# Performance work log

Hardware: AMD Instinct MI355X
Metric: run time of the kernel (lower is better)

The kernel has to match this reference:

```python
import jax, jax.numpy as jnp
import numpy as np

B, D, L = 4, 512, 4096
N1, N2 = 1167, 8921


def setup_inputs() -> dict:
    key = jax.random.key(0)
    k1, k2, k3, k4 = jax.random.split(key, 4)
    H = jax.random.normal(k1, (B, D, L), dtype=jnp.float32)
    Q1_w = jax.random.normal(k2, (N1, D), dtype=jnp.float32) * (1.0 / np.sqrt(D))
    Q2_w = jax.random.normal(k3, (N2, D), dtype=jnp.float32) * (1.0 / np.sqrt(D))
    Q12_w = jax.random.normal(k4, (N2, N1), dtype=jnp.float32) * (1.0 / np.sqrt(N1))
    return {"H": H, "Q1_w": Q1_w, "Q2_w": Q2_w, "Q12_w": Q12_w}


def reference(H, Q1_w, Q2_w, Q12_w):
    # H: [b, d, l]; Q1_w: [n1, d]; Q2_w: [n2, d]; Q12_w: [n2, n1]
    # Level-1 label attention
    E1 = jnp.einsum('nd,bdl->bnl', Q1_w, H)          # [b, n1, l]
    A1 = jax.nn.softmax(E1, axis=2)
    C1 = jnp.einsum('bnl,bdl->bnd', A1, H)           # [b, n1, d]
    # Project level-1 context to level-2 label space
    C1 = jnp.einsum('mn,bnd->bmd', Q12_w, C1)        # [b, n2, d]
    # Level-2 queries modulated by level-1 context (elementwise)
    Q2 = Q2_w[None, :, :] * C1                       # [b, n2, d]
    E2 = jnp.einsum('bmd,bdl->bml', Q2, H)           # [b, n2, l]
    A2 = jax.nn.softmax(E2, axis=2)
    C2 = jnp.einsum('bml,bdl->bmd', A2, H)           # [b, n2, d]
    return (C2, A2)
```

## Files before the change

kernel.cpp:

```cpp
#include <hip/hip_runtime.h>
#include <hip/hip_bf16.h>

typedef __bf16 bf16_t;
typedef __bf16 bf16x8 __attribute__((ext_vector_type(8)));
typedef __bf16 bf16x4 __attribute__((ext_vector_type(4)));
typedef float  f32x4  __attribute__((ext_vector_type(4)));

#define BM 128
#define BN 128
#define BK 64

#define SBAR() asm volatile("s_barrier" ::: "memory")

__global__ __launch_bounds__(256) void cast_transpose_H(
    const float* __restrict__ H, bf16_t* __restrict__ Hb,
    bf16_t* __restrict__ HTb, int D, int L) {
  __shared__ bf16_t tile[32][33];
  int b = blockIdx.z;
  int l0 = blockIdx.x * 32, d0 = blockIdx.y * 32;
  const float* Hp = H + (size_t)b * D * L;
  bf16_t* Hbp = Hb + (size_t)b * D * L;
  bf16_t* HTp = HTb + (size_t)b * L * D;
  int tx = threadIdx.x, ty = threadIdx.y;
#pragma unroll
  for (int r = 0; r < 4; r++) {
    int d = d0 + ty + r * 8;
    float v = Hp[(size_t)d * L + l0 + tx];
    bf16_t bv = (bf16_t)v;
    tile[ty + r * 8][tx] = bv;
    Hbp[(size_t)d * L + l0 + tx] = bv;
  }
  __syncthreads();
#pragma unroll
  for (int r = 0; r < 4; r++) {
    int l = l0 + ty + r * 8;
    HTp[(size_t)l * D + d0 + tx] = tile[tx][ty + r * 8];
  }
}

__global__ void cast_w(const float* __restrict__ in, bf16_t* __restrict__ out, int n) {
  int i = blockIdx.x * 256 + threadIdx.x;
  if (i < n) out[i] = (bf16_t)in[i];
}

__global__ void cast_w_pad(const float* __restrict__ in, bf16_t* __restrict__ out,
                           int cols, int ldo) {
  int c = blockIdx.x * 256 + threadIdx.x;
  int r = blockIdx.y;
  if (c < ldo) {
    float v = (c < cols) ? in[(size_t)r * cols + c] : 0.0f;
    out[(size_t)r * ldo + c] = (bf16_t)v;
  }
}

__global__ void zero_rows(bf16_t* __restrict__ p, int r0, int nr, long sb, int L) {
  long i = (long)blockIdx.x * 256 + threadIdx.x;
  int b = blockIdx.y;
  long tot = (long)nr * L / 8;
  if (i < tot) {
    bf16x8 z = {};
    *(bf16x8*)(p + ((long)b * sb + r0) * L + i * 8) = z;
  }
}

__device__ inline bf16x8 cvt8(float4 a, float4 b) {
  bf16x8 o;
  o[0] = (bf16_t)a.x; o[1] = (bf16_t)a.y; o[2] = (bf16_t)a.z; o[3] = (bf16_t)a.w;
  o[4] = (bf16_t)b.x; o[5] = (bf16_t)b.y; o[6] = (bf16_t)b.z; o[7] = (bf16_t)b.w;
  return o;
}

__device__ inline void gload_lds16(const bf16_t* g, bf16_t* l) {
  __builtin_amdgcn_global_load_lds(
      (const __attribute__((address_space(1))) void*)g,
      (__attribute__((address_space(3))) void*)l, 16, 0, 0);
}

__device__ inline void stage_half(const bf16_t* __restrict__ src, int ld,
                                  bf16_t* lds_half, int t, int wid) {
  int r = t >> 3;
  int gsl = (t & 7) ^ (r & 7);
  const bf16_t* g = src + (size_t)r * ld + gsl * 8;
  gload_lds16(g, lds_half + wid * 512);
  gload_lds16(g + (size_t)64 * ld, lds_half + 4096 + wid * 512);
}

template <int EPI>
__global__ __launch_bounds__(512) void gemm256_bt(
    const bf16_t* __restrict__ A, long sAb, const bf16_t* __restrict__ BT, long sBb,
    void* __restrict__ Cv, long sCb, const float* __restrict__ W,
    int M, int N, int K, int lda, int ldb, int ldc) {
  __shared__ __align__(16) bf16_t As[2][256][64];
  __shared__ __align__(16) bf16_t Bs[2][256][64];
  int b = blockIdx.z;
  A += (size_t)b * sAb;
  BT += (size_t)b * sBb;

  int nx = gridDim.x, ny = gridDim.y;
  int nwg = nx * ny;
  int bid = blockIdx.x + nx * blockIdx.y;
  int qq = nwg >> 3, rr = nwg & 7;
  int xcd = bid & 7, lin = bid >> 3;
  int swz = (xcd < rr ? xcd * (qq + 1) : rr * (qq + 1) + (xcd - rr) * qq) + lin;
  int m0 = (swz / ny) * 256;
  int n0 = (swz % ny) * 256;

  int t = threadIdx.x;
  int lane = t & 63, wid = t >> 6;
  int l15 = lane & 15, q = lane >> 4;
  int wm = (wid >> 2) * 128;
  int wn = (wid & 3) * 64;
  int NT = K >> 6;

  f32x4 acc[8][4];
#pragma unroll
  for (int i = 0; i < 8; i++)
#pragma unroll
    for (int j = 0; j < 4; j++)
#pragma unroll
      for (int e = 0; e < 4; e++) acc[i][j][e] = 0.0f;

  stage_half(BT + (size_t)(n0 + 0) * ldb, ldb, &Bs[0][0][0], t, wid);
  stage_half(BT + (size_t)(n0 + 128) * ldb, ldb, &Bs[0][128][0], t, wid);
  stage_half(A + (size_t)(m0 + 0) * lda, lda, &As[0][0][0], t, wid);
  stage_half(A + (size_t)(m0 + 128) * lda, lda, &As[0][128][0], t, wid);
  stage_half(BT + (size_t)(n0 + 0) * ldb + 64, ldb, &Bs[1][0][0], t, wid);
  stage_half(BT + (size_t)(n0 + 128) * ldb + 64, ldb, &Bs[1][128][0], t, wid);
  asm volatile("s_waitcnt vmcnt(4)" ::: "memory");
  SBAR();

  bf16x8 af[4][2];
  bf16x8 bF[2][2][2];

  for (int kt = 0; kt < NT; ++kt) {
    int buf = kt & 1;
    const bf16_t* An = A + (size_t)m0 * lda + (size_t)(kt + 1) * 64;
    const bf16_t* Bn2 = BT + (size_t)n0 * ldb + (size_t)(kt + 2) * 64;

    auto readA = [&](int mh) {
#pragma unroll
      for (int i = 0; i < 4; i++) {
        const char* rowp = (const char*)&As[buf][wm + mh * 64 + i * 16 + l15][0];
#pragma unroll
        for (int ks = 0; ks < 2; ks++)
          af[i][ks] = *(const bf16x8*)(rowp + ((((ks * 4 + q) ^ (l15 & 7))) << 4));
      }
    };
    auto readB = [&](int ch) {
#pragma unroll
      for (int j = 0; j < 2; j++) {
        const char* rowp = (const char*)&Bs[buf][wn + ch * 32 + j * 16 + l15][0];
#pragma unroll
        for (int ks = 0; ks < 2; ks++)
          bF[ch][j][ks] = *(const bf16x8*)(rowp + ((((ks * 4 + q) ^ (l15 & 7))) << 4));
      }
    };
    auto mmaq = [&](int mh, int ch) {
      __builtin_amdgcn_s_setprio(1);
#pragma unroll
      for (int i = 0; i < 4; i++)
#pragma unroll
        for (int j = 0; j < 2; j++)
#pragma unroll
          for (int ks = 0; ks < 2; ks++)
            acc[mh * 4 + i][ch * 2 + j] = __builtin_amdgcn_mfma_f32_16x16x32_bf16(
                af[i][ks], bF[ch][j][ks], acc[mh * 4 + i][ch * 2 + j], 0, 0, 0);
      __builtin_amdgcn_s_setprio(0);
    };

    readA(0);
    readB(0);
    if (kt + 1 < NT) stage_half(An, lda, &As[buf ^ 1][0][0], t, wid);
    SBAR();
    mmaq(0, 0);
    SBAR();
    readB(1);
    if (kt + 1 < NT) stage_half(An + (size_t)128 * lda, lda, &As[buf ^ 1][128][0], t, wid);
    SBAR();
    mmaq(0, 1);
    SBAR();
    readA(1);
    if (kt + 2 < NT) stage_half(Bn2, ldb, &Bs[buf][0][0], t, wid);
    SBAR();
    mmaq(1, 0);
    SBAR();
    if (kt + 2 < NT) {
      stage_half(Bn2 + (size_t)128 * ldb, ldb, &Bs[buf][128][0], t, wid);
      asm volatile("s_waitcnt vmcnt(4)" ::: "memory");
    } else if (kt + 1 < NT) {
      asm volatile("s_waitcnt vmcnt(0)" ::: "memory");
    }
    SBAR();
    mmaq(1, 1);
    SBAR();
  }

#pragma unroll
  for (int ig = 0; ig < 8; ig++) {
    int rbase = m0 + wm + ig * 16 + q * 4;
#pragma unroll
    for (int jg = 0; jg < 4; jg++) {
      int c = n0 + wn + jg * 16 + l15;
#pragma unroll
      for (int r4 = 0; r4 < 4; r4++) {
        int r = rbase + r4;
        if (r < M) {
          float val = acc[ig][jg][r4];
          ((float*)Cv + (size_t)b * sCb)[(size_t)r * ldc + c] = val;
        }
      }
    }
  }
}

template <typename AT, int EPI>
__global__ __launch_bounds__(256) void gemm_bt(
    const AT* __restrict__ A, long sAb, const bf16_t* __restrict__ BT, long sBb,
    void* __restrict__ Cv, long sCb, const float* __restrict__ W,
    int M, int N, int K, int lda, int ldb, int ldc) {
  constexpr bool AF32 = (sizeof(AT) == 4);
  __shared__ __align__(16) bf16_t As[BM][BK];
  __shared__ __align__(16) bf16_t Bs[BN][BK];
  int b = blockIdx.z;
  A += (size_t)b * sAb;
  BT += (size_t)b * sBb;

  int nx = gridDim.x, ny = gridDim.y;
  int nwg = nx * ny;
  int bid = blockIdx.x + nx * blockIdx.y;
  int qq = nwg >> 3, rr = nwg & 7;
  int xcd = bid & 7, lin = bid >> 3;
  int swz = (xcd < rr ? xcd * (qq + 1) : rr * (qq + 1) + (xcd - rr) * qq) + lin;
  int m0 = (swz / ny) * BM;
  int n0 = (swz % ny) * BN;

  int t = threadIdx.x;
  int lane = t & 63, wid = t >> 6;
  int l15 = lane & 15, q = lane >> 4;
  int wm = (wid >> 1) * 64, wn = (wid & 1) * 64;

  int r0 = t >> 3;
  int sl = t & 7;
  int gsl = sl ^ (r0 & 7);
  bf16_t* lA = &As[0][0] + (size_t)wid * 512;
  bf16_t* lB = &Bs[0][0] + (size_t)wid * 512;

  f32x4 acc[4][4];
#pragma unroll
  for (int i = 0; i < 4; i++)
#pragma unroll
    for (int j = 0; j < 4; j++)
#pragma unroll
      for (int e = 0; e < 4; e++) acc[i][j][e] = 0.0f;

  for (int kb = 0; kb < K; kb += BK) {
    float4 va[4][2];
    if constexpr (AF32) {
#pragma unroll
      for (int i = 0; i < 4; i++) {
        int gm = m0 + i * 32 + r0;
        if (gm < M) {
          const float4* p = (const float4*)(A + (size_t)gm * lda + kb + gsl * 8);
          va[i][0] = p[0];
          va[i][1] = p[1];
        } else {
          va[i][0] = make_float4(0.f, 0.f, 0.f, 0.f);
          va[i][1] = make_float4(0.f, 0.f, 0.f, 0.f);
        }
      }
    }
    __syncthreads();
#pragma unroll
    for (int i = 0; i < 4; i++)
      gload_lds16(BT + (size_t)(n0 + i * 32 + r0) * ldb + kb + gsl * 8,
                  lB + i * 2048);
    if constexpr (AF32) {
#pragma unroll
      for (int i = 0; i < 4; i++)
        *(bf16x8*)(&As[0][0] + (size_t)(i * 256 + t) * 8) = cvt8(va[i][0], va[i][1]);
    } else {
#pragma unroll
      for (int i = 0; i < 4; i++)
        gload_lds16(A + (size_t)(m0 + i * 32 + r0) * lda + kb + gsl * 8,
                    lA + i * 2048);
    }
    __syncthreads();

#pragma unroll
    for (int ks = 0; ks < 2; ks++) {
      bf16x8 af[4], bfr[4];
#pragma unroll
      for (int i = 0; i < 4; i++) {
        int row = wm + i * 16 + l15;
        int off = (ks * 64 + q * 16) ^ ((l15 & 7) << 4);
        af[i] = *(const bf16x8*)((const char*)&As[row][0] + off);
      }
#pragma unroll
      for (int j = 0; j < 4; j++) {
        int row = wn + j * 16 + l15;
        int off = (ks * 64 + q * 16) ^ ((l15 & 7) << 4);
        bfr[j] = *(const bf16x8*)((const char*)&Bs[row][0] + off);
      }
#pragma unroll
      for (int i = 0; i < 4; i++)
#pragma unroll
        for (int j = 0; j < 4; j++)
          acc[i][j] = __builtin_amdgcn_mfma_f32_16x16x32_bf16(af[i], bfr[j],
                                                              acc[i][j], 0, 0, 0);
    }
  }

#pragma unroll
  for (int i = 0; i < 4; i++) {
    int rbase = m0 + wm + i * 16 + q * 4;
#pragma unroll
    for (int j = 0; j < 4; j++) {
      int c = n0 + wn + j * 16 + l15;
#pragma unroll
      for (int r4 = 0; r4 < 4; r4++) {
        int r = rbase + r4;
        if (r < M) {
          float val = acc[i][j][r4];
          if (EPI == 0) {
            float* Cp = (float*)Cv + (size_t)b * sCb;
            Cp[(size_t)r * ldc + c] = val;
          } else if (EPI == 2) {
            float w = W[(size_t)r * N + c];
            bf16_t* Cp = (bf16_t*)Cv + (size_t)b * sCb;
            Cp[(size_t)r * ldc + c] = (bf16_t)(val * w);
          } else {
            bf16_t* Cp = (bf16_t*)Cv + (size_t)b * sCb;
            Cp[(size_t)r * ldc + c] = (bf16_t)val;
          }
        }
      }
    }
  }
}

template <int MODE>
__global__ __launch_bounds__(256) void softmax_rows(
    const float* __restrict__ in, void* __restrict__ out,
    bf16_t* __restrict__ out2, int L, int ostr) {
  long row_in = (long)blockIdx.y * gridDim.x + blockIdx.x;
  long row_out = (long)blockIdx.y * ostr + blockIdx.x;
  const float* ip = in + row_in * L;
  int t = threadIdx.x;
  int lane = t & 63, wid = t >> 6;
  float4 v[4];
  float m = -3.4e38f;
#pragma unroll
  for (int c = 0; c < 4; c++) {
    v[c] = ((const float4*)ip)[c * 256 + t];
    m = fmaxf(m, fmaxf(fmaxf(v[c].x, v[c].y), fmaxf(v[c].z, v[c].w)));
  }
#pragma unroll
  for (int off = 1; off < 64; off <<= 1) m = fmaxf(m, __shfl_xor(m, off));
  __shared__ float redm[4];
  __shared__ float reds[4];
  if (lane == 0) redm[wid] = m;
  __syncthreads();
  m = fmaxf(fmaxf(redm[0], redm[1]), fmaxf(redm[2], redm[3]));
  float s = 0.0f;
#pragma unroll
  for (int c = 0; c < 4; c++) {
    v[c].x = __expf(v[c].x - m);
    v[c].y = __expf(v[c].y - m);
    v[c].z = __expf(v[c].z - m);
    v[c].w = __expf(v[c].w - m);
    s += (v[c].x + v[c].y) + (v[c].z + v[c].w);
  }
#pragma unroll
  for (int off = 1; off < 64; off <<= 1) s += __shfl_xor(s, off);
  if (lane == 0) reds[wid] = s;
  __syncthreads();
  s = (reds[0] + reds[1]) + (reds[2] + reds[3]);
  float inv = 1.0f / s;
  if (MODE == 1) {
    bf16_t* op = (bf16_t*)out + row_out * L;
#pragma unroll
    for (int c = 0; c < 4; c++) {
      bf16x4 o;
      o[0] = (bf16_t)(v[c].x * inv);
      o[1] = (bf16_t)(v[c].y * inv);
      o[2] = (bf16_t)(v[c].z * inv);
      o[3] = (bf16_t)(v[c].w * inv);
      *(bf16x4*)(op + ((size_t)c * 256 + t) * 4) = o;
    }
  } else {
    float* op = (float*)out + row_out * L;
#pragma unroll
    for (int c = 0; c < 4; c++) {
      float fx = v[c].x * inv, fy = v[c].y * inv, fz = v[c].z * inv, fw = v[c].w * inv;
      ((float4*)op)[c * 256 + t] = make_float4(fx, fy, fz, fw);
      if (MODE == 2) {
        bf16x4 o;
        o[0] = (bf16_t)fx; o[1] = (bf16_t)fy; o[2] = (bf16_t)fz; o[3] = (bf16_t)fw;
        *(bf16x4*)(out2 + row_out * L + ((size_t)c * 256 + t) * 4) = o;
      }
    }
  }
}

extern "C" void kernel_launch(void* const* d_in, const int* in_sizes, int n_in,
                              void* d_out, int out_size, void* d_ws, size_t ws_size,
                              hipStream_t stream) {
  const int B = 4, D = 512, L = 4096, N1 = 1167, N2 = 8921;
  const int N1P = 1280;
  const int M2P = 8960;
  const float* H = (const float*)d_in[0];
  const float* Q1w = (const float*)d_in[1];
  const float* Q2w = (const float*)d_in[2];
  const float* Q12w = (const float*)d_in[3];
  float* C2 = (float*)d_out;
  float* A2 = C2 + (size_t)B * N2 * D;

  char* ws = (char*)d_ws;
  size_t off = 0;
  auto alloc = [&](size_t bytes) -> void* {
    void* p = ws + off;
    off = (off + bytes + 255) & ~(size_t)255;
    return p;
  };
  bf16_t* Hb   = (bf16_t*)alloc((size_t)B * D * L * 2);
  bf16_t* HTb  = (bf16_t*)alloc((size_t)B * L * D * 2);
  bf16_t* Q1b  = (bf16_t*)alloc((size_t)N1P * D * 2);
  bf16_t* Q12b = (bf16_t*)alloc((size_t)M2P * N1P * 2);
  float*  E1   = (float*)alloc((size_t)B * N1 * L * 4);
  bf16_t* A1b  = (bf16_t*)alloc((size_t)B * N1P * L * 2);
  bf16_t* C1Tb = (bf16_t*)alloc((size_t)B * D * N1P * 2);
  bf16_t* Q2b  = (bf16_t*)alloc(((size_t)B * N2 + 64) * D * 2);
  size_t a2b_bytes = ((size_t)B * N2 + 128) * (size_t)L * 2;
  bool useA2b = (ws_size > 0) && (off + a2b_bytes <= ws_size);
  bf16_t* A2b = (bf16_t*)alloc(a2b_bytes);

  cast_transpose_H<<<dim3(L / 32, D / 32, B), dim3(32, 8), 0, stream>>>(H, Hb, HTb, D, L);
  cast_w_pad<<<dim3((D + 255) / 256, N1P), 256, 0, stream>>>(Q1w, Q1b, D, D);
  zero_rows<<<dim3(((N1P - N1) * D / 8 + 255) / 256, 1), 256, 0, stream>>>(
      Q1b, N1, N1P - N1, 0, D);
  cast_w_pad<<<dim3((N1P + 255) / 256, N2), 256, 0, stream>>>(Q12w, Q12b, N1, N1P);
  zero_rows<<<dim3(((N1P - N1) * L / 8 + 255) / 256, B), 256, 0, stream>>>(
      A1b, N1, N1P - N1, (long)N1P, L);
  gemm_bt<bf16_t, 0><<<dim3(N1P / BM, L / BN, B), 256, 0, stream>>>(
      Q1b, 0, HTb, (long)L * D, E1, (long)N1 * L, nullptr, N1, L, D, D, D, L);
  softmax_rows<1><<<dim3(N1, B), 256, 0, stream>>>(E1, A1b, nullptr, L, N1P);
  gemm_bt<bf16_t, 3><<<dim3(D / BM, N1P / BN, B), 256, 0, stream>>>(
      Hb, (long)D * L, A1b, (long)N1P * L, C1Tb, (long)D * N1P, nullptr,
      D, N1P, L, L, L, N1P);
  gemm_bt<bf16_t, 2><<<dim3(M2P / BM, D / BN, B), 256, 0, stream>>>(
      Q12b, 0, C1Tb, (long)D * N1P, Q2b, (long)N2 * D, Q2w, N2, D, N1P, N1P, N1P, D);
  gemm256_bt<0><<<dim3(M2P / 256, L / 256, B), 512, 0, stream>>>(
      Q2b, (long)N2 * D, HTb, (long)L * D, A2, (long)N2 * L, nullptr, N2, L, D, D, D, L);
  if (useA2b) {
    softmax_rows<2><<<dim3(B * N2, 1), 256, 0, stream>>>(A2, A2, A2b, L, 0);
    gemm_bt<bf16_t, 0><<<dim3(M2P / BM, D / BN, B), 256, 0, stream>>>(
        A2b, (long)N2 * L, Hb, (long)D * L, C2, (long)N2 * D, nullptr, N2, D, L, L, L, D);
  } else {
    softmax_rows<0><<<dim3(B * N2, 1), 256, 0, stream>>>(A2, A2, nullptr, L, 0);
    gemm_bt<float, 0><<<dim3(M2P / BM, D / BN, B), 256, 0, stream>>>(
        A2, (long)N2 * L, Hb, (long)D * L, C2, (long)N2 * D, nullptr, N2, D, L, L, L, D);
  }
}
```

Measured before the change: 1.649 ms.

## Use nontemporal stores/loads for A2 path and trim padded K in Q12 GEMM

Switches the large fp32 E2/A2 stores in the 256-tile GEMM and the MODE 2 softmax loads and stores to nontemporal variants, so streaming data does not pollute the cache. Reduces the K extent of the Q12 projection GEMM from the padded 1280 to 1216, skipping all-zero padding columns. Also casts only the real Q1 rows instead of the padded count and removes an unused kernel. Nontemporal hints can hurt if the A2 data would have been re-read from cache by the following softmax.

```diff
diff --git a/kernel.cpp b/kernel.cpp
--- a/kernel.cpp
+++ b/kernel.cpp
@@ -38,11 +38,6 @@
   }
 }
 
-__global__ void cast_w(const float* __restrict__ in, bf16_t* __restrict__ out, int n) {
-  int i = blockIdx.x * 256 + threadIdx.x;
-  if (i < n) out[i] = (bf16_t)in[i];
-}
-
 __global__ void cast_w_pad(const float* __restrict__ in, bf16_t* __restrict__ out,
                            int cols, int ldo) {
   int c = blockIdx.x * 256 + threadIdx.x;
@@ -206,7 +201,8 @@
         int r = rbase + r4;
         if (r < M) {
           float val = acc[ig][jg][r4];
-          ((float*)Cv + (size_t)b * sCb)[(size_t)r * ldc + c] = val;
+          float* Cp = (float*)Cv + (size_t)b * sCb;
+          __builtin_nontemporal_store(val, &Cp[(size_t)r * ldc + c]);
         }
       }
     }
@@ -347,12 +343,15 @@
   const float* ip = in + row_in * L;
   int t = threadIdx.x;
   int lane = t & 63, wid = t >> 6;
-  float4 v[4];
+  f32x4 v[4];
   float m = -3.4e38f;
 #pragma unroll
   for (int c = 0; c < 4; c++) {
-    v[c] = ((const float4*)ip)[c * 256 + t];
-    m = fmaxf(m, fmaxf(fmaxf(v[c].x, v[c].y), fmaxf(v[c].z, v[c].w)));
+    if (MODE == 2)
+      v[c] = __builtin_nontemporal_load((const f32x4*)ip + c * 256 + t);
+    else
+      v[c] = ((const f32x4*)ip)[c * 256 + t];
+    m = fmaxf(m, fmaxf(fmaxf(v[c][0], v[c][1]), fmaxf(v[c][2], v[c][3])));
   }
 #pragma unroll
   for (int off = 1; off < 64; off <<= 1) m = fmaxf(m, __shfl_xor(m, off));
@@ -364,11 +363,11 @@
   float s = 0.0f;
 #pragma unroll
   for (int c = 0; c < 4; c++) {
-    v[c].x = __expf(v[c].x - m);
-    v[c].y = __expf(v[c].y - m);
-    v[c].z = __expf(v[c].z - m);
-    v[c].w = __expf(v[c].w - m);
-    s += (v[c].x + v[c].y) + (v[c].z + v[c].w);
+    v[c][0] = __expf(v[c][0] - m);
+    v[c][1] = __expf(v[c][1] - m);
+    v[c][2] = __expf(v[c][2] - m);
+    v[c][3] = __expf(v[c][3] - m);
+    s += (v[c][0] + v[c][1]) + (v[c][2] + v[c][3]);
   }
 #pragma unroll
   for (int off = 1; off < 64; off <<= 1) s += __shfl_xor(s, off);
@@ -381,22 +380,25 @@
 #pragma unroll
     for (int c = 0; c < 4; c++) {
       bf16x4 o;
-      o[0] = (bf16_t)(v[c].x * inv);
-      o[1] = (bf16_t)(v[c].y * inv);
-      o[2] = (bf16_t)(v[c].z * inv);
-      o[3] = (bf16_t)(v[c].w * inv);
+      o[0] = (bf16_t)(v[c][0] * inv);
+      o[1] = (bf16_t)(v[c][1] * inv);
+      o[2] = (bf16_t)(v[c][2] * inv);
+      o[3] = (bf16_t)(v[c][3] * inv);
       *(bf16x4*)(op + ((size_t)c * 256 + t) * 4) = o;
     }
   } else {
     float* op = (float*)out + row_out * L;
 #pragma unroll
     for (int c = 0; c < 4; c++) {
-      float fx = v[c].x * inv, fy = v[c].y * inv, fz = v[c].z * inv, fw = v[c].w * inv;
-      ((float4*)op)[c * 256 + t] = make_float4(fx, fy, fz, fw);
+      f32x4 o = v[c] * inv;
       if (MODE == 2) {
-        bf16x4 o;
-        o[0] = (bf16_t)fx; o[1] = (bf16_t)fy; o[2] = (bf16_t)fz; o[3] = (bf16_t)fw;
-        *(bf16x4*)(out2 + row_out * L + ((size_t)c * 256 + t) * 4) = o;
+        __builtin_nontemporal_store(o, (f32x4*)op + c * 256 + t);
+        bf16x4 ob;
+        ob[0] = (bf16_t)o[0]; ob[1] = (bf16_t)o[1];
+        ob[2] = (bf16_t)o[2]; ob[3] = (bf16_t)o[3];
+        __builtin_nontemporal_store(ob, (bf16x4*)(out2 + row_out * L) + c * 256 + t);
+      } else {
+        ((f32x4*)op)[c * 256 + t] = o;
       }
     }
   }
@@ -407,6 +409,7 @@
                               hipStream_t stream) {
   const int B = 4, D = 512, L = 4096, N1 = 1167, N2 = 8921;
   const int N1P = 1280;
+  const int N1K = 1216;
   const int M2P = 8960;
   const float* H = (const float*)d_in[0];
   const float* Q1w = (const float*)d_in[1];
@@ -435,7 +438,7 @@
   bf16_t* A2b = (bf16_t*)alloc(a2b_bytes);
 
   cast_transpose_H<<<dim3(L / 32, D / 32, B), dim3(32, 8), 0, stream>>>(H, Hb, HTb, D, L);
-  cast_w_pad<<<dim3((D + 255) / 256, N1P), 256, 0, stream>>>(Q1w, Q1b, D, D);
+  cast_w_pad<<<dim3((D + 255) / 256, N1), 256, 0, stream>>>(Q1w, Q1b, D, D);
   zero_rows<<<dim3(((N1P - N1) * D / 8 + 255) / 256, 1), 256, 0, stream>>>(
       Q1b, N1, N1P - N1, 0, D);
   cast_w_pad<<<dim3((N1P + 255) / 256, N2), 256, 0, stream>>>(Q12w, Q12b, N1, N1P);
@@ -448,7 +451,7 @@
       Hb, (long)D * L, A1b, (long)N1P * L, C1Tb, (long)D * N1P, nullptr,
       D, N1P, L, L, L, N1P);
   gemm_bt<bf16_t, 2><<<dim3(M2P / BM, D / BN, B), 256, 0, stream>>>(
-      Q12b, 0, C1Tb, (long)D * N1P, Q2b, (long)N2 * D, Q2w, N2, D, N1P, N1P, N1P, D);
+      Q12b, 0, C1Tb, (long)D * N1P, Q2b, (long)N2 * D, Q2w, N2, D, N1K, N1P, N1P, D);
   gemm256_bt<0><<<dim3(M2P / 256, L / 256, B), 512, 0, stream>>>(
       Q2b, (long)N2 * D, HTb, (long)L * D, A2, (long)N2 * L, nullptr, N2, L, D, D, D, L);
   if (useA2b) {
```

Result: no change. 1.631 ms (-1.1%).
